# Kernel optimization log

Hardware: AMD Instinct MI355X
Metric: run time of the kernel (lower is better)

Reference implementation:

```python
import jax, jax.numpy as jnp
import numpy as np
import math

N_HEADS = 16
D_EMBED = 1024
D_CROSS = 768
FF_DIM = 4096
D_HEAD = D_EMBED // N_HEADS
LN_EPS = 1e-5


def layer_norm(h, g, b):
    mu = jnp.mean(h, axis=-1, keepdims=True)
    var = jnp.var(h, axis=-1, keepdims=True)
    return (h - mu) * jax.lax.rsqrt(var + LN_EPS) * g + b


def mha(q, k, v):
    # q: [B,Sq,D], k/v: [B,Skv,D] -> split heads, attend, merge
    B, Sq, _ = q.shape
    Skv = k.shape[1]
    qh = q.reshape(B, Sq, N_HEADS, D_HEAD).transpose(0, 2, 1, 3)
    kh = k.reshape(B, Skv, N_HEADS, D_HEAD).transpose(0, 2, 1, 3)
    vh = v.reshape(B, Skv, N_HEADS, D_HEAD).transpose(0, 2, 1, 3)
    scores = jnp.einsum('bhqd,bhkd->bhqk', qh, kh) / math.sqrt(D_HEAD)
    attn = jax.nn.softmax(scores, axis=-1)
    out = jnp.einsum('bhqk,bhkd->bhqd', attn, vh)
    return out.transpose(0, 2, 1, 3).reshape(B, Sq, D_EMBED)


def setup_inputs() -> dict:
    key = jax.random.key(0)
    ks = jax.random.split(key, 24)
    s = 0.02
    inp = {
        'x': jax.random.normal(ks[0], (4, 1024, D_EMBED), jnp.float32),
        'y': jax.random.normal(ks[1], (4, 77, D_CROSS), jnp.float32),
        # self-attention in_proj (d_embed -> 3*d_embed) and out_proj
        'w_qkv': jax.random.normal(ks[2], (D_EMBED, 3 * D_EMBED), jnp.float32) * s,
        'b_qkv': jnp.zeros((3 * D_EMBED,), jnp.float32),
        'w_so': jax.random.normal(ks[3], (D_EMBED, D_EMBED), jnp.float32) * s,
        'b_so': jnp.zeros((D_EMBED,), jnp.float32),
        # cross-attention projections
        'w_q': jax.random.normal(ks[4], (D_EMBED, D_EMBED), jnp.float32) * s,
        'b_q': jnp.zeros((D_EMBED,), jnp.float32),
        'w_k': jax.random.normal(ks[5], (D_CROSS, D_EMBED), jnp.float32) * s,
        'b_k': jnp.zeros((D_EMBED,), jnp.float32),
        'w_v': jax.random.normal(ks[6], (D_CROSS, D_EMBED), jnp.float32) * s,
        'b_v': jnp.zeros((D_EMBED,), jnp.float32),
        'w_co': jax.random.normal(ks[7], (D_EMBED, D_EMBED), jnp.float32) * s,
        'b_co': jnp.zeros((D_EMBED,), jnp.float32),
        # 3-layer FFN
        'w1': jax.random.normal(ks[8], (D_EMBED, FF_DIM), jnp.float32) * s,
        'b1': jnp.zeros((FF_DIM,), jnp.float32),
        'w2': jax.random.normal(ks[9], (FF_DIM, FF_DIM), jnp.float32) * s,
        'b2': jnp.zeros((FF_DIM,), jnp.float32),
        'w3': jax.random.normal(ks[10], (FF_DIM, D_EMBED), jnp.float32) * s,
        'b3': jnp.zeros((D_EMBED,), jnp.float32),
        # single shared LayerNorm (used 3 times, as in the torch module)
        'ln_g': jnp.ones((D_EMBED,), jnp.float32),
        'ln_b': jnp.zeros((D_EMBED,), jnp.float32),
    }
    return inp


def reference(x, y, w_qkv, b_qkv, w_so, b_so, w_q, b_q, w_k, b_k, w_v, b_v,
              w_co, b_co, w1, b1, w2, b2, w3, b3, ln_g, ln_b):
    # --- self attention (no causal mask) ---
    qkv = x @ w_qkv + b_qkv
    q, k, v = jnp.split(qkv, 3, axis=-1)
    sa = mha(q, k, v) @ w_so + b_so
    x = layer_norm(x + sa, ln_g, ln_b)
    # --- cross attention ---
    qc = x @ w_q + b_q
    kc = y @ w_k + b_k
    vc = y @ w_v + b_v
    ca = mha(qc, kc, vc) @ w_co + b_co
    x = layer_norm(x + ca, ln_g, ln_b)
    # --- 3-layer FFN with ReLU ---
    h = jax.nn.relu(x @ w1 + b1)
    h = jax.nn.relu(h @ w2 + b2)
    ff = h @ w3 + b3
    x = layer_norm(x + ff, ln_g, ln_b)
    return x
```

## Files before the change

### kernel.cpp

```cpp
#include <hip/hip_runtime.h>
#include <hip/hip_bf16.h>
#include <math.h>

typedef short v8s __attribute__((ext_vector_type(8)));
typedef short v4s __attribute__((ext_vector_type(4)));
typedef float v4f __attribute__((ext_vector_type(4)));

__device__ __forceinline__ unsigned short f2bf(float f) {
  union { float f; unsigned u; } a; a.f = f;
  unsigned u = a.u + 0x7fffu + ((a.u >> 16) & 1u);
  return (unsigned short)(u >> 16);
}

__device__ __forceinline__ void gld_lds16(const unsigned short* g, unsigned short* l) {
  __builtin_amdgcn_global_load_lds(
      (const __attribute__((address_space(1))) void*)g,
      (__attribute__((address_space(3))) void*)l,
      16, 0, 0);
}

#define VMCNT(n)  asm volatile("s_waitcnt vmcnt(" #n ")" ::: "memory")
#define LGKM(n)   asm volatile("s_waitcnt lgkmcnt(" #n ")" ::: "memory")

__global__ void cvt_f32_bf16(const float* __restrict__ in,
                             unsigned short* __restrict__ out, int n4) {
  int i = blockIdx.x * blockDim.x + threadIdx.x;
  if (i >= n4) return;
  float4 v = reinterpret_cast<const float4*>(in)[i];
  ushort4 o;
  o.x = f2bf(v.x); o.y = f2bf(v.y); o.z = f2bf(v.z); o.w = f2bf(v.w);
  reinterpret_cast<ushort4*>(out)[i] = o;
}

__global__ void cvt_transpose(const float* __restrict__ in,
                              unsigned short* __restrict__ out, int K, int N) {
  __shared__ float t[32][33];
  int bx = blockIdx.x, by = blockIdx.y;
  int tx = threadIdx.x, ty = threadIdx.y;
#pragma unroll
  for (int i = 0; i < 4; i++) {
    int k = by * 32 + ty + i * 8;
    t[ty + i * 8][tx] = in[(size_t)k * N + bx * 32 + tx];
  }
  __syncthreads();
#pragma unroll
  for (int i = 0; i < 4; i++) {
    int n = bx * 32 + ty + i * 8;
    out[(size_t)n * K + by * 32 + tx] = f2bf(t[tx][ty + i * 8]);
  }
}

__global__ __launch_bounds__(256)
void transpose_v(const unsigned short* __restrict__ V,
                 unsigned short* __restrict__ Vt,
                 int rowstride, int batch_rows, int Skv, int kvpad) {
  __shared__ __align__(16) unsigned short t[64][80];
  int ch = blockIdx.x, h = blockIdx.y, b = blockIdx.z;
  int tid = threadIdx.x;
  int sr = tid >> 2, sc = (tid & 3) * 16;
  int gr = ch * 64 + sr;
  v8s v0 = {}, v1 = {};
  if (gr < Skv) {
    const unsigned short* p = V + (size_t)(b * batch_rows + gr) * rowstride + h * 64 + sc;
    v0 = *(const v8s*)p; v1 = *(const v8s*)(p + 8);
  }
  *(v8s*)&t[sr][sc]     = v0;
  *(v8s*)&t[sr][sc + 8] = v1;
  __syncthreads();
  int d  = tid >> 2;
  int k0 = (tid & 3) * 16;
  unsigned short* o = Vt + ((size_t)(b * 16 + h) * 64 + d) * kvpad + ch * 64 + k0;
  v8s o0, o1;
#pragma unroll
  for (int e = 0; e < 8; e++) { o0[e] = t[k0 + e][d]; o1[e] = t[k0 + 8 + e][d]; }
  *(v8s*)o       = o0;
  *(v8s*)(o + 8) = o1;
}

#define PH_MFMA(AFR, IB, JB)                                                   \
  _Pragma("unroll")                                                            \
  for (int m = 0; m < 4; m++) {                                                \
    _Pragma("unroll")                                                          \
    for (int n = 0; n < 2; n++) {                                              \
      acc[IB + m][JB + n] = __builtin_amdgcn_mfma_f32_16x16x32_bf16(           \
          AFR[m][0], bF[n][0], acc[IB + m][JB + n], 0, 0, 0);                  \
      acc[IB + m][JB + n] = __builtin_amdgcn_mfma_f32_16x16x32_bf16(           \
          AFR[m][1], bF[n][1], acc[IB + m][JB + n], 0, 0, 0);                  \
    }                                                                          \
  }

template<bool RELU>
__global__ __launch_bounds__(512, 2)
void gemm256(const unsigned short* __restrict__ A,
             const unsigned short* __restrict__ BT,
             const float* __restrict__ bias,
             unsigned short* __restrict__ Cb,
             int M, int N, int K, int lda, int ldb) {
  __shared__ __align__(16) unsigned short lA[2][2][8192];
  __shared__ __align__(16) unsigned short lB[2][2][8192];
  int tid  = threadIdx.x;
  int lane = tid & 63;
  int wave = tid >> 6;
  int wrow = wave >> 2;
  int wcol = wave & 3;
  int quad = lane >> 4;
  int l15  = lane & 15;
  int m0 = blockIdx.y * 256;
  int n0 = blockIdx.x * 256;
  int NT = K >> 6;

  int lrow = lane >> 3;
  int swz8 = ((lane & 7) ^ lrow) << 3;
  const unsigned short* gA0 = A + (size_t)(m0 + wave * 8 + lrow) * lda + swz8;
  int rr = wave * 8 + lrow;
  int nbase = (rr >> 5) * 64 + (rr & 31);
  const unsigned short* gB0 = BT + (size_t)(n0 + nbase) * ldb + swz8;

  auto stageA = [&](int U, int h, int rlo) {
    unsigned short* d = &lA[U & 1][h][(rlo + wave * 8) * 64];
    gld_lds16(gA0 + (size_t)(h * 128 + rlo) * lda + (size_t)U * 64, d);
  };
  auto stageB = [&](int U, int hB, int q) {
    unsigned short* d = &lB[U & 1][hB][(q * 64 + wave * 8) * 64];
    gld_lds16(gB0 + (size_t)(q * 128 + hB * 32) * ldb + (size_t)U * 64, d);
  };

  int ch0 = (quad ^ (l15 & 7)) << 3;
  int ch1 = ch0 ^ 32;
  int wcol32 = wcol * 32;

  const v4f vzero = {0.f, 0.f, 0.f, 0.f};
  v4f acc[8][4];
#pragma unroll
  for (int i = 0; i < 8; i++)
#pragma unroll
    for (int j = 0; j < 4; j++) acc[i][j] = vzero;

  v8s aF0[4][2], aF1[4][2], bF[2][2];

  stageA(0, 0, 0);  stageA(0, 1, 0);
  stageB(0, 0, 0);  stageB(0, 0, 1);
  stageA(0, 0, 64); stageA(0, 1, 64);
  stageB(0, 1, 0);  stageB(0, 1, 1);
  if (NT > 1) {
    stageA(1, 0, 0);  stageA(1, 1, 0);
    stageB(1, 0, 0);  stageB(1, 0, 1);
    stageA(1, 0, 64); stageA(1, 1, 64);
    VMCNT(8);
  } else {
    VMCNT(0);
  }
  __builtin_amdgcn_s_barrier();

  for (int U = 0; U < NT; ++U) {
    int c = U & 1;
    bool tail = (U + 3 >= NT);
    const unsigned short* pA  = &lA[c][wrow][0];
    const unsigned short* pB0 = &lB[c][0][0];
    const unsigned short* pB1 = &lB[c][1][0];

#pragma unroll
    for (int m = 0; m < 4; m++) {
      int ro = (m * 16 + l15) * 64;
      aF0[m][0] = *(const v8s*)&pA[ro + ch0];
      aF0[m][1] = *(const v8s*)&pA[ro + ch1];
    }
#pragma unroll
    for (int n = 0; n < 2; n++) {
      int ro = (wcol32 + n * 16 + l15) * 64;
      bF[n][0] = *(const v8s*)&pB0[ro + ch0];
      bF[n][1] = *(const v8s*)&pB0[ro + ch1];
    }
    if (U + 1 < NT) { stageB(U + 1, 1, 0); stageB(U + 1, 1, 1); }
    LGKM(8);
    __builtin_amdgcn_s_barrier();
    LGKM(0);
    __builtin_amdgcn_sched_barrier(0);
    __builtin_amdgcn_s_setprio(1);
    PH_MFMA(aF0, 0, 0)
    __builtin_amdgcn_s_setprio(0);
    __builtin_amdgcn_s_barrier();

#pragma unroll
    for (int m = 0; m < 4; m++) {
      int ro = (64 * 64) + (m * 16 + l15) * 64;
      aF1[m][0] = *(const v8s*)&pA[ro + ch0];
      aF1[m][1] = *(const v8s*)&pA[ro + ch1];
    }
    if (U + 2 < NT) { stageA(U + 2, 0, 0); stageA(U + 2, 1, 0); }
    __builtin_amdgcn_s_barrier();
    LGKM(0);
    __builtin_amdgcn_sched_barrier(0);
    __builtin_amdgcn_s_setprio(1);
    PH_MFMA(aF1, 4, 0)
    __builtin_amdgcn_s_setprio(0);
    if (tail) { VMCNT(0); } else { VMCNT(10); }
    __builtin_amdgcn_s_barrier();

#pragma unroll
    for (int n = 0; n < 2; n++) {
      int ro = (wcol32 + n * 16 + l15) * 64;
      bF[n][0] = *(const v8s*)&pB1[ro + ch0];
      bF[n][1] = *(const v8s*)&pB1[ro + ch1];
    }
    if (U + 2 < NT) { stageB(U + 2, 0, 0); stageB(U + 2, 0, 1); }
    __builtin_amdgcn_s_barrier();
    LGKM(0);
    __builtin_amdgcn_sched_barrier(0);
    __builtin_amdgcn_s_setprio(1);
    PH_MFMA(aF1, 4, 2)
    __builtin_amdgcn_s_setprio(0);
    __builtin_amdgcn_s_barrier();

    if (U + 2 < NT) { stageA(U + 2, 0, 64); stageA(U + 2, 1, 64); }
    __builtin_amdgcn_s_barrier();
    __builtin_amdgcn_s_setprio(1);
    PH_MFMA(aF0, 0, 2)
    __builtin_amdgcn_s_setprio(0);
    if (tail) { VMCNT(0); } else { VMCNT(8); }
    __builtin_amdgcn_s_barrier();
  }

#pragma unroll
  for (int j = 0; j < 4; j++) {
    int col = n0 + wcol * 64 + (j >> 1) * 32 + (j & 1) * 16 + l15;
    float bv = bias[col];
#pragma unroll
    for (int i = 0; i < 8; i++) {
      int rb = m0 + wrow * 128 + (i >> 2) * 64 + (i & 3) * 16 + quad * 4;
#pragma unroll
      for (int r = 0; r < 4; r++) {
        int row = rb + r;
        if (row < M) {
          float v = acc[i][j][r] + bv;
          if (RELU) v = fmaxf(v, 0.f);
          Cb[(size_t)row * N + col] = f2bf(v);
        }
      }
    }
  }
}

template<bool RELU, bool OUTF, bool OUTB>
__global__ __launch_bounds__(256)
void gemm_bf16(const unsigned short* __restrict__ A,
               const unsigned short* __restrict__ BT,
               const float* __restrict__ bias,
               float* __restrict__ Cf, float* __restrict__ Cf2,
               unsigned short* __restrict__ Cb,
               int M, int N, int Kred, int ld) {
  __shared__ __align__(16) unsigned short lA[128 * 64];
  __shared__ __align__(16) unsigned short lB[128 * 64];
  int tid  = threadIdx.x;
  int lane = tid & 63;
  int wave = tid >> 6;
  int wr = (wave >> 1) * 64;
  int wc = (wave & 1) * 64;
  int quad = lane >> 4;
  int l15  = lane & 15;
  int m0 = blockIdx.y * 128;
  int n0 = blockIdx.x * 128;
  int z  = blockIdx.z;

  const unsigned short* Az = A  + (size_t)z * Kred;
  const unsigned short* Bz = BT + (size_t)z * Kred;
  float* Cfo = z ? Cf2 : Cf;
  const float* biasz = z ? nullptr : bias;

  int srow   = tid >> 3;
  int schunk = (tid & 7) ^ (srow & 7);
  const unsigned short* gA = Az + (size_t)(m0 + srow) * ld + schunk * 8;
  const unsigned short* gB = Bz + (size_t)(n0 + srow) * ld + schunk * 8;
  unsigned short* ldsA = lA + wave * 512;
  unsigned short* ldsB = lB + wave * 512;
  const size_t rowblk = (size_t)32 * ld;

  const v4f vzero = {0.f, 0.f, 0.f, 0.f};
  v4f acc[4][4];
#pragma unroll
  for (int i = 0; i < 4; i++)
#pragma unroll
    for (int j = 0; j < 4; j++) acc[i][j] = vzero;

  for (int k0 = 0; k0 < Kred; k0 += 64) {
#pragma unroll
    for (int i = 0; i < 4; i++) {
      gld_lds16(gA + k0 + i * rowblk, ldsA + i * 2048);
      gld_lds16(gB + k0 + i * rowblk, ldsB + i * 2048);
    }
    __syncthreads();
#pragma unroll
    for (int s = 0; s < 2; s++) {
      v8s aF[4], bF[4];
#pragma unroll
      for (int i = 0; i < 4; i++)
        aF[i] = *(const v8s*)&lA[(wr + i * 16 + l15) * 64 + (((s * 4 + quad) ^ (l15 & 7)) * 8)];
#pragma unroll
      for (int j = 0; j < 4; j++)
        bF[j] = *(const v8s*)&lB[(wc + j * 16 + l15) * 64 + (((s * 4 + quad) ^ (l15 & 7)) * 8)];
#pragma unroll
      for (int i = 0; i < 4; i++)
#pragma unroll
        for (int j = 0; j < 4; j++)
          acc[i][j] = __builtin_amdgcn_mfma_f32_16x16x32_bf16(aF[i], bF[j], acc[i][j], 0, 0, 0);
    }
    __syncthreads();
  }

#pragma unroll
  for (int j = 0; j < 4; j++) {
    int col = n0 + wc + j * 16 + l15;
    float bv = biasz ? biasz[col] : 0.f;
#pragma unroll
    for (int i = 0; i < 4; i++) {
#pragma unroll
      for (int r = 0; r < 4; r++) {
        int row = m0 + wr + i * 16 + quad * 4 + r;
        if (row < M) {
          float v = acc[i][j][r] + bv;
          if (RELU) v = fmaxf(v, 0.f);
          if (OUTF) Cfo[(size_t)row * N + col] = v;
          if (OUTB && !z) Cb[(size_t)row * N + col] = f2bf(v);
        }
      }
    }
  }
}

__global__ __launch_bounds__(256)
void attn_kernel(const unsigned short* __restrict__ Q,
                 const unsigned short* __restrict__ K,
                 const unsigned short* __restrict__ Vt,
                 unsigned short* __restrict__ O,
                 int q_rowstride, int kv_rowstride, int o_rowstride,
                 int q_batch_rows, int kv_batch_rows, int Skv, int kvpad,
                 float scale) {
  __shared__ __align__(16) unsigned short lK[64][72];
  __shared__ __align__(16) unsigned short lV[64][72];
  __shared__ __align__(16) unsigned short lP[4][16][72];
  int tid  = threadIdx.x;
  int lane = tid & 63;
  int wave = tid >> 6;
  int quad = lane >> 4;
  int l15  = lane & 15;
  int qt = blockIdx.x, h = blockIdx.y, b = blockIdx.z;

  const unsigned short* Qb  = Q  + (size_t)b * q_batch_rows * q_rowstride + h * 64;
  const unsigned short* Kb  = K  + (size_t)b * kv_batch_rows * kv_rowstride + h * 64;
  const unsigned short* Vtb = Vt + ((size_t)(b * 16 + h) * 64) * kvpad;

  v8s qf0, qf1;
  {
    const unsigned short* qr = Qb + (size_t)(qt * 64 + wave * 16 + l15) * q_rowstride + quad * 8;
    qf0 = *(const v8s*)(qr);
    qf1 = *(const v8s*)(qr + 32);
  }

  const v4f vzero = {0.f, 0.f, 0.f, 0.f};
  v4f o_acc[4];
#pragma unroll
  for (int t = 0; t < 4; t++) o_acc[t] = vzero;
  float m_r[4], l_r[4];
#pragma unroll
  for (int r = 0; r < 4; r++) { m_r[r] = -1e30f; l_r[r] = 0.f; }

  int sr = tid >> 2;
  int sc = (tid & 3) * 16;

  int nch = (Skv + 63) >> 6;
  for (int ch = 0; ch < nch; ch++) {
    int base = ch * 64;
    int gr = base + sr;
    v8s k0v = {}, k1v = {};
    if (gr < Skv) {
      const unsigned short* kp = Kb + (size_t)gr * kv_rowstride + sc;
      k0v = *(const v8s*)kp;  k1v = *(const v8s*)(kp + 8);
    }
    const unsigned short* vp = Vtb + (size_t)sr * kvpad + base + sc;
    v8s w0 = *(const v8s*)vp;
    v8s w1 = *(const v8s*)(vp + 8);
    __syncthreads();
    *(v8s*)&lK[sr][sc]     = k0v;
    *(v8s*)&lK[sr][sc + 8] = k1v;
    {
      v4s a0 = {w0[0], w0[1], w0[2], w0[3]};
      v4s a1 = {w0[4], w0[5], w0[6], w0[7]};
      v4s a2 = {w1[0], w1[1], w1[2], w1[3]};
      v4s a3 = {w1[4], w1[5], w1[6], w1[7]};
      *(v4s*)&lV[sr][sc]      = a0;
      *(v4s*)&lV[sr][sc + 4]  = a1;
      *(v4s*)&lV[sr][sc + 8]  = a2;
      *(v4s*)&lV[sr][sc + 12] = a3;
    }
    __syncthreads();

    float s[4][4];
#pragma unroll
    for (int t = 0; t < 4; t++) {
      v8s kf0 = *(const v8s*)&lK[t * 16 + l15][quad * 8];
      v8s kf1 = *(const v8s*)&lK[t * 16 + l15][32 + quad * 8];
      v4f sacc = vzero;
      sacc = __builtin_amdgcn_mfma_f32_16x16x32_bf16(qf0, kf0, sacc, 0, 0, 0);
      sacc = __builtin_amdgcn_mfma_f32_16x16x32_bf16(qf1, kf1, sacc, 0, 0, 0);
      int kvpos = base + t * 16 + l15;
      bool ok = kvpos < Skv;
#pragma unroll
      for (int r = 0; r < 4; r++) s[t][r] = ok ? sacc[r] * scale : -1e30f;
    }

#pragma unroll
    for (int r = 0; r < 4; r++) {
      float mx = fmaxf(fmaxf(s[0][r], s[1][r]), fmaxf(s[2][r], s[3][r]));
#pragma unroll
      for (int d = 1; d < 16; d <<= 1) mx = fmaxf(mx, __shfl_xor(mx, d));
      float mnew = fmaxf(m_r[r], mx);
      float alpha = __expf(m_r[r] - mnew);
      float sm = 0.f;
#pragma unroll
      for (int t = 0; t < 4; t++) { s[t][r] = __expf(s[t][r] - mnew); sm += s[t][r]; }
#pragma unroll
      for (int d = 1; d < 16; d <<= 1) sm += __shfl_xor(sm, d);
      l_r[r] = l_r[r] * alpha + sm;
      m_r[r] = mnew;
#pragma unroll
      for (int t = 0; t < 4; t++) o_acc[t][r] *= alpha;
    }

#pragma unroll
    for (int t = 0; t < 4; t++)
#pragma unroll
      for (int r = 0; r < 4; r++)
        lP[wave][quad * 4 + r][t * 16 + l15] = f2bf(s[t][r]);
    v8s pf0 = *(const v8s*)&lP[wave][l15][quad * 8];
    v8s pf1 = *(const v8s*)&lP[wave][l15][32 + quad * 8];
#pragma unroll
    for (int t = 0; t < 4; t++) {
      v8s vf0 = *(const v8s*)&lV[t * 16 + l15][quad * 8];
      v8s vf1 = *(const v8s*)&lV[t * 16 + l15][32 + quad * 8];
      o_acc[t] = __builtin_amdgcn_mfma_f32_16x16x32_bf16(pf0, vf0, o_acc[t], 0, 0, 0);
      o_acc[t] = __builtin_amdgcn_mfma_f32_16x16x32_bf16(pf1, vf1, o_acc[t], 0, 0, 0);
    }
  }

  int orow0 = b * q_batch_rows + qt * 64 + wave * 16;
#pragma unroll
  for (int t = 0; t < 4; t++) {
#pragma unroll
    for (int r = 0; r < 4; r++) {
      float v = o_acc[t][r] / l_r[r];
      O[(size_t)(orow0 + quad * 4 + r) * o_rowstride + h * 64 + t * 16 + l15] = f2bf(v);
    }
  }
}

__global__ __launch_bounds__(256)
void ln_kernel(const float* base, const float* __restrict__ delta,
               const float* __restrict__ delta2,
               const float* __restrict__ g, const float* __restrict__ bb,
               float* outf, unsigned short* __restrict__ outb) {
  __shared__ float red[8];
  int row = blockIdx.x;
  int tid = threadIdx.x;
  float4 vb = ((const float4*)(base  + (size_t)row * 1024))[tid];
  float4 vd = ((const float4*)(delta + (size_t)row * 1024))[tid];
  float v0 = vb.x + vd.x, v1 = vb.y + vd.y, v2 = vb.z + vd.z, v3 = vb.w + vd.w;
  if (delta2) {
    float4 v2d = ((const float4*)(delta2 + (size_t)row * 1024))[tid];
    v0 += v2d.x; v1 += v2d.y; v2 += v2d.z; v3 += v2d.w;
  }
  float s = v0 + v1 + v2 + v3;
  float q = v0 * v0 + v1 * v1 + v2 * v2 + v3 * v3;
#pragma unroll
  for (int d = 1; d < 64; d <<= 1) { s += __shfl_xor(s, d); q += __shfl_xor(q, d); }
  int wave = tid >> 6, lane = tid & 63;
  if (lane == 0) { red[wave] = s; red[4 + wave] = q; }
  __syncthreads();
  s = red[0] + red[1] + red[2] + red[3];
  q = red[4] + red[5] + red[6] + red[7];
  float mean = s * (1.f / 1024.f);
  float var  = q * (1.f / 1024.f) - mean * mean;
  float rstd = rsqrtf(var + 1e-5f);
  float4 gg  = ((const float4*)g)[tid];
  float4 bv  = ((const float4*)bb)[tid];
  float o0 = (v0 - mean) * rstd * gg.x + bv.x;
  float o1 = (v1 - mean) * rstd * gg.y + bv.y;
  float o2 = (v2 - mean) * rstd * gg.z + bv.z;
  float o3 = (v3 - mean) * rstd * gg.w + bv.w;
  if (outf) {
    float4 o; o.x = o0; o.y = o1; o.z = o2; o.w = o3;
    ((float4*)(outf + (size_t)row * 1024))[tid] = o;
  }
  if (outb) {
    ushort4 u; u.x = f2bf(o0); u.y = f2bf(o1); u.z = f2bf(o2); u.w = f2bf(o3);
    ((ushort4*)(outb + (size_t)row * 1024))[tid] = u;
  }
}

extern "C" void kernel_launch(void* const* d_in, const int* in_sizes, int n_in,
                              void* d_out, int out_size, void* d_ws, size_t ws_size,
                              hipStream_t stream) {
  const float* x     = (const float*)d_in[0];
  const float* y     = (const float*)d_in[1];
  const float* w_qkv = (const float*)d_in[2];
  const float* b_qkv = (const float*)d_in[3];
  const float* w_so  = (const float*)d_in[4];
  const float* b_so  = (const float*)d_in[5];
  const float* w_q   = (const float*)d_in[6];
  const float* b_q   = (const float*)d_in[7];
  const float* w_k   = (const float*)d_in[8];
  const float* b_k   = (const float*)d_in[9];
  const float* w_v   = (const float*)d_in[10];
  const float* b_v   = (const float*)d_in[11];
  const float* w_co  = (const float*)d_in[12];
  const float* b_co  = (const float*)d_in[13];
  const float* w1    = (const float*)d_in[14];
  const float* b1    = (const float*)d_in[15];
  const float* w2    = (const float*)d_in[16];
  const float* b2    = (const float*)d_in[17];
  const float* w3    = (const float*)d_in[18];
  const float* b3    = (const float*)d_in[19];
  const float* ln_g  = (const float*)d_in[20];
  const float* ln_b  = (const float*)d_in[21];

  char* ws = (char*)d_ws;
  auto US = [&](size_t off) { return (unsigned short*)(ws + off); };
  auto FP = [&](size_t off) { return (float*)(ws + off); };

  constexpr size_t o_wqkv = 0;
  constexpr size_t o_wso  = o_wqkv + 3072ull * 1024 * 2;
  constexpr size_t o_wq   = o_wso  + 1024ull * 1024 * 2;
  constexpr size_t o_wk   = o_wq   + 1024ull * 1024 * 2;
  constexpr size_t o_wv   = o_wk   + 1024ull * 768 * 2;
  constexpr size_t o_wco  = o_wv   + 1024ull * 768 * 2;
  constexpr size_t o_w1   = o_wco  + 1024ull * 1024 * 2;
  constexpr size_t o_w2   = o_w1   + 4096ull * 1024 * 2;
  constexpr size_t o_w3   = o_w2   + 4096ull * 4096 * 2;
  constexpr size_t o_xf   = o_w3   + 1024ull * 4096 * 2;
  constexpr size_t o_xbf  = o_xf   + 4096ull * 1024 * 4;
  constexpr size_t o_ybf  = o_xbf  + 4096ull * 1024 * 2;
  constexpr size_t o_dlt  = o_ybf  + 308ull * 768 * 2;
  constexpr size_t o_R1   = o_dlt  + 4096ull * 1024 * 4;
  constexpr size_t o_attn = o_R1   + 4096ull * 3072 * 2;
  constexpr size_t o_R2   = o_attn + 4096ull * 1024 * 2;
  constexpr size_t o_qc  = o_R1;
  constexpr size_t o_kc  = o_R1 + 4096ull * 1024 * 2;
  constexpr size_t o_vc  = o_kc + 308ull * 1024 * 2;
  constexpr size_t o_h1  = o_R1;
  constexpr size_t o_h2  = o_R2;
  constexpr size_t o_dlt2 = o_R1;
  constexpr size_t o_vtS = o_R2;
  constexpr size_t o_vtC = o_R2 + 4ull * 16 * 64 * 1024 * 2;

  dim3 tb(32, 8);
  cvt_transpose<<<dim3(96, 32),  tb, 0, stream>>>(w_qkv, US(o_wqkv), 1024, 3072);
  cvt_transpose<<<dim3(32, 32),  tb, 0, stream>>>(w_so,  US(o_wso),  1024, 1024);
  cvt_transpose<<<dim3(32, 32),  tb, 0, stream>>>(w_q,   US(o_wq),   1024, 1024);
  cvt_transpose<<<dim3(32, 24),  tb, 0, stream>>>(w_k,   US(o_wk),   768,  1024);
  cvt_transpose<<<dim3(32, 24),  tb, 0, stream>>>(w_v,   US(o_wv),   768,  1024);
  cvt_transpose<<<dim3(32, 32),  tb, 0, stream>>>(w_co,  US(o_wco),  1024, 1024);
  cvt_transpose<<<dim3(128, 32), tb, 0, stream>>>(w1,    US(o_w1),   1024, 4096);
  cvt_transpose<<<dim3(128, 128),tb, 0, stream>>>(w2,    US(o_w2),   4096, 4096);
  cvt_transpose<<<dim3(32, 128), tb, 0, stream>>>(w3,    US(o_w3),   4096, 1024);

  cvt_f32_bf16<<<4096, 256, 0, stream>>>(x, US(o_xbf), 4096 * 1024 / 4);
  cvt_f32_bf16<<<231, 256, 0, stream>>>(y, US(o_ybf), 4 * 77 * 768 / 4);

  gemm256<false><<<dim3(12, 16), 512, 0, stream>>>(
      US(o_xbf), US(o_wqkv), b_qkv, US(o_R1), 4096, 3072, 1024, 1024, 1024);
  transpose_v<<<dim3(16, 16, 4), 256, 0, stream>>>(
      US(o_R1) + 2048, US(o_vtS), 3072, 1024, 1024, 1024);
  attn_kernel<<<dim3(16, 16, 4), 256, 0, stream>>>(
      US(o_R1), US(o_R1) + 1024, US(o_vtS), US(o_attn),
      3072, 3072, 1024, 1024, 1024, 1024, 1024, 0.125f);
  gemm_bf16<false, true, false><<<dim3(8, 32, 2), 256, 0, stream>>>(
      US(o_attn), US(o_wso), b_so, FP(o_dlt), FP(o_dlt2), nullptr, 4096, 1024, 512, 1024);
  ln_kernel<<<4096, 256, 0, stream>>>(x, FP(o_dlt), FP(o_dlt2), ln_g, ln_b,
                                      FP(o_xf), US(o_xbf));

  gemm_bf16<false, false, true><<<dim3(8, 32, 1), 256, 0, stream>>>(
      US(o_xbf), US(o_wq), b_q, nullptr, nullptr, US(o_qc), 4096, 1024, 1024, 1024);
  gemm_bf16<false, false, true><<<dim3(8, 3, 1), 256, 0, stream>>>(
      US(o_ybf), US(o_wk), b_k, nullptr, nullptr, US(o_kc), 308, 1024, 768, 768);
  gemm_bf16<false, false, true><<<dim3(8, 3, 1), 256, 0, stream>>>(
      US(o_ybf), US(o_wv), b_v, nullptr, nullptr, US(o_vc), 308, 1024, 768, 768);
  transpose_v<<<dim3(2, 16, 4), 256, 0, stream>>>(
      US(o_vc), US(o_vtC), 1024, 77, 77, 128);
  attn_kernel<<<dim3(16, 16, 4), 256, 0, stream>>>(
      US(o_qc), US(o_kc), US(o_vtC), US(o_attn),
      1024, 1024, 1024, 1024, 77, 77, 128, 0.125f);
  gemm_bf16<false, true, false><<<dim3(8, 32, 2), 256, 0, stream>>>(
      US(o_attn), US(o_wco), b_co, FP(o_dlt), FP(o_dlt2), nullptr, 4096, 1024, 512, 1024);
  ln_kernel<<<4096, 256, 0, stream>>>(FP(o_xf), FP(o_dlt), FP(o_dlt2), ln_g, ln_b,
                                      FP(o_xf), US(o_xbf));

  gemm256<true><<<dim3(16, 16), 512, 0, stream>>>(
      US(o_xbf), US(o_w1), b1, US(o_h1), 4096, 4096, 1024, 1024, 1024);
  gemm256<true><<<dim3(16, 16), 512, 0, stream>>>(
      US(o_h1), US(o_w2), b2, US(o_h2), 4096, 4096, 4096, 4096, 4096);
  gemm_bf16<false, true, false><<<dim3(8, 32, 2), 256, 0, stream>>>(
      US(o_h2), US(o_w3), b3, FP(o_dlt), FP(o_dlt2), nullptr, 4096, 1024, 2048, 4096);
  ln_kernel<<<4096, 256, 0, stream>>>(FP(o_xf), FP(o_dlt), FP(o_dlt2), ln_g, ln_b,
                                      (float*)d_out, nullptr);
}
```

Measured before the change: 754.3 us.

## Prefetch next K/V chunk in attention and fuse cross K/V projections

The attention loop now loads the next 64-row K and V chunk into registers while the current chunk is being computed, so global-load latency overlaps the MFMA work. The two `__syncthreads` are replaced by raw `s_barrier` calls with explicit lgkmcnt waits and scheduling barriers. Separately, the cross-attention K and V projections become one GEMM with N=2048. This works because the transposed `w_k` and `w_v` are contiguous in memory, and a split bias pointer handles the second half. The trade-offs are higher register pressure in the attention kernel and reliance on the fixed weight layout.

```diff
diff --git a/kernel.cpp b/kernel.cpp
--- a/kernel.cpp
+++ b/kernel.cpp
@@ -246,6 +246,7 @@
 void gemm_bf16(const unsigned short* __restrict__ A,
                const unsigned short* __restrict__ BT,
                const float* __restrict__ bias,
+               const float* __restrict__ bias2, int bsplit,
                float* __restrict__ Cf, float* __restrict__ Cf2,
                unsigned short* __restrict__ Cb,
                int M, int N, int Kred, int ld) {
@@ -310,7 +311,8 @@
 #pragma unroll
   for (int j = 0; j < 4; j++) {
     int col = n0 + wc + j * 16 + l15;
-    float bv = biasz ? biasz[col] : 0.f;
+    float bv = 0.f;
+    if (biasz) bv = (bias2 && col >= bsplit) ? bias2[col - bsplit] : biasz[col];
 #pragma unroll
     for (int i = 0; i < 4; i++) {
 #pragma unroll
@@ -366,33 +368,47 @@
 
   int sr = tid >> 2;
   int sc = (tid & 3) * 16;
-
   int nch = (Skv + 63) >> 6;
+
+  v8s kv0 = {}, kv1 = {}, vv0, vv1;
+  if (sr < Skv) {
+    const unsigned short* kp = Kb + (size_t)sr * kv_rowstride + sc;
+    kv0 = *(const v8s*)kp;  kv1 = *(const v8s*)(kp + 8);
+  }
+  {
+    const unsigned short* vp = Vtb + (size_t)sr * kvpad + sc;
+    vv0 = *(const v8s*)vp;  vv1 = *(const v8s*)(vp + 8);
+  }
+
   for (int ch = 0; ch < nch; ch++) {
     int base = ch * 64;
-    int gr = base + sr;
-    v8s k0v = {}, k1v = {};
-    if (gr < Skv) {
-      const unsigned short* kp = Kb + (size_t)gr * kv_rowstride + sc;
-      k0v = *(const v8s*)kp;  k1v = *(const v8s*)(kp + 8);
-    }
-    const unsigned short* vp = Vtb + (size_t)sr * kvpad + base + sc;
-    v8s w0 = *(const v8s*)vp;
-    v8s w1 = *(const v8s*)(vp + 8);
-    __syncthreads();
-    *(v8s*)&lK[sr][sc]     = k0v;
-    *(v8s*)&lK[sr][sc + 8] = k1v;
+    __builtin_amdgcn_s_barrier();
+    __builtin_amdgcn_sched_barrier(0);
+    *(v8s*)&lK[sr][sc]     = kv0;
+    *(v8s*)&lK[sr][sc + 8] = kv1;
     {
-      v4s a0 = {w0[0], w0[1], w0[2], w0[3]};
-      v4s a1 = {w0[4], w0[5], w0[6], w0[7]};
-      v4s a2 = {w1[0], w1[1], w1[2], w1[3]};
-      v4s a3 = {w1[4], w1[5], w1[6], w1[7]};
+      v4s a0 = {vv0[0], vv0[1], vv0[2], vv0[3]};
+      v4s a1 = {vv0[4], vv0[5], vv0[6], vv0[7]};
+      v4s a2 = {vv1[0], vv1[1], vv1[2], vv1[3]};
+      v4s a3 = {vv1[4], vv1[5], vv1[6], vv1[7]};
       *(v4s*)&lV[sr][sc]      = a0;
       *(v4s*)&lV[sr][sc + 4]  = a1;
       *(v4s*)&lV[sr][sc + 8]  = a2;
       *(v4s*)&lV[sr][sc + 12] = a3;
     }
-    __syncthreads();
+    v8s kn0 = {}, kn1 = {}, vn0 = {}, vn1 = {};
+    if (ch + 1 < nch) {
+      int gr2 = base + 64 + sr;
+      if (gr2 < Skv) {
+        const unsigned short* kp2 = Kb + (size_t)gr2 * kv_rowstride + sc;
+        kn0 = *(const v8s*)kp2;  kn1 = *(const v8s*)(kp2 + 8);
+      }
+      const unsigned short* vp2 = Vtb + (size_t)sr * kvpad + base + 64 + sc;
+      vn0 = *(const v8s*)vp2;  vn1 = *(const v8s*)(vp2 + 8);
+    }
+    LGKM(0);
+    __builtin_amdgcn_s_barrier();
+    __builtin_amdgcn_sched_barrier(0);
 
     float s[4][4];
 #pragma unroll
@@ -440,6 +456,8 @@
       o_acc[t] = __builtin_amdgcn_mfma_f32_16x16x32_bf16(pf0, vf0, o_acc[t], 0, 0, 0);
       o_acc[t] = __builtin_amdgcn_mfma_f32_16x16x32_bf16(pf1, vf1, o_acc[t], 0, 0, 0);
     }
+
+    kv0 = kn0; kv1 = kn1; vv0 = vn0; vv1 = vn1;
   }
 
   int orow0 = b * q_batch_rows + qt * 64 + wave * 16;
@@ -544,7 +562,6 @@
   constexpr size_t o_R2   = o_attn + 4096ull * 1024 * 2;
   constexpr size_t o_qc  = o_R1;
   constexpr size_t o_kc  = o_R1 + 4096ull * 1024 * 2;
-  constexpr size_t o_vc  = o_kc + 308ull * 1024 * 2;
   constexpr size_t o_h1  = o_R1;
   constexpr size_t o_h2  = o_R2;
   constexpr size_t o_dlt2 = o_R1;
@@ -573,23 +590,25 @@
       US(o_R1), US(o_R1) + 1024, US(o_vtS), US(o_attn),
       3072, 3072, 1024, 1024, 1024, 1024, 1024, 0.125f);
   gemm_bf16<false, true, false><<<dim3(8, 32, 2), 256, 0, stream>>>(
-      US(o_attn), US(o_wso), b_so, FP(o_dlt), FP(o_dlt2), nullptr, 4096, 1024, 512, 1024);
+      US(o_attn), US(o_wso), b_so, nullptr, 0,
+      FP(o_dlt), FP(o_dlt2), nullptr, 4096, 1024, 512, 1024);
   ln_kernel<<<4096, 256, 0, stream>>>(x, FP(o_dlt), FP(o_dlt2), ln_g, ln_b,
                                       FP(o_xf), US(o_xbf));
 
   gemm_bf16<false, false, true><<<dim3(8, 32, 1), 256, 0, stream>>>(
-      US(o_xbf), US(o_wq), b_q, nullptr, nullptr, US(o_qc), 4096, 1024, 1024, 1024);
-  gemm_bf16<false, false, true><<<dim3(8, 3, 1), 256, 0, stream>>>(
-      US(o_ybf), US(o_wk), b_k, nullptr, nullptr, US(o_kc), 308, 1024, 768, 768);
-  gemm_bf16<false, false, true><<<dim3(8, 3, 1), 256, 0, stream>>>(
-      US(o_ybf), US(o_wv), b_v, nullptr, nullptr, US(o_vc), 308, 1024, 768, 768);
+      US(o_xbf), US(o_wq), b_q, nullptr, 0,
+      nullptr, nullptr, US(o_qc), 4096, 1024, 1024, 1024);
+  gemm_bf16<false, false, true><<<dim3(16, 3, 1), 256, 0, stream>>>(
+      US(o_ybf), US(o_wk), b_k, b_v, 1024,
+      nullptr, nullptr, US(o_kc), 308, 2048, 768, 768);
   transpose_v<<<dim3(2, 16, 4), 256, 0, stream>>>(
-      US(o_vc), US(o_vtC), 1024, 77, 77, 128);
+      US(o_kc) + 1024, US(o_vtC), 2048, 77, 77, 128);
   attn_kernel<<<dim3(16, 16, 4), 256, 0, stream>>>(
       US(o_qc), US(o_kc), US(o_vtC), US(o_attn),
-      1024, 1024, 1024, 1024, 77, 77, 128, 0.125f);
+      1024, 2048, 1024, 1024, 77, 77, 128, 0.125f);
   gemm_bf16<false, true, false><<<dim3(8, 32, 2), 256, 0, stream>>>(
-      US(o_attn), US(o_wco), b_co, FP(o_dlt), FP(o_dlt2), nullptr, 4096, 1024, 512, 1024);
+      US(o_attn), US(o_wco), b_co, nullptr, 0,
+      FP(o_dlt), FP(o_dlt2), nullptr, 4096, 1024, 512, 1024);
   ln_kernel<<<4096, 256, 0, stream>>>(FP(o_xf), FP(o_dlt), FP(o_dlt2), ln_g, ln_b,
                                       FP(o_xf), US(o_xbf));
 
@@ -598,7 +617,8 @@
   gemm256<true><<<dim3(16, 16), 512, 0, stream>>>(
       US(o_h1), US(o_w2), b2, US(o_h2), 4096, 4096, 4096, 4096, 4096);
   gemm_bf16<false, true, false><<<dim3(8, 32, 2), 256, 0, stream>>>(
-      US(o_h2), US(o_w3), b3, FP(o_dlt), FP(o_dlt2), nullptr, 4096, 1024, 2048, 4096);
+      US(o_h2), US(o_w3), b3, nullptr, 0,
+      FP(o_dlt), FP(o_dlt2), nullptr, 4096, 1024, 2048, 4096);
   ln_kernel<<<4096, 256, 0, stream>>>(FP(o_xf), FP(o_dlt), FP(o_dlt2), ln_g, ln_b,
                                       (float*)d_out, nullptr);
 }
```

Measured after the change: 735.9 us. 2.4% less time.
